# Kernel optimization log

Measured on AMD Instinct MI355X. Metric: run time of the kernel, lower is better.

Reference implementation:

```python
import jax, jax.numpy as jnp
import numpy as np

N_RAYS = 262144
N_BINS = 64          # bin edges per ray
N_IMPORTANCE = 128   # fine samples per ray


def setup_inputs() -> dict:
    key = jax.random.key(0)
    k1, k2, k3 = jax.random.split(key, 3)
    # bins must be sorted along last axis (bin edges): cumsum of positive steps
    steps = jax.random.uniform(k1, (N_RAYS, N_BINS), dtype=jnp.float32) + 0.01
    bins = jnp.cumsum(steps, axis=-1)
    weights = jax.random.uniform(k2, (N_RAYS, N_BINS - 1), dtype=jnp.float32)
    # u plays the role of torch.rand t_vals (deterministic=False path)
    u = jax.random.uniform(k3, (N_RAYS, N_IMPORTANCE), dtype=jnp.float32)
    return {"bins": bins, "weights": weights, "u": u, "n_importance": N_IMPORTANCE}


def reference(bins, weights, u, n_importance):
    # weights: [N, M-1]; bins: [N, M]; u: [N, n_importance]
    weights = weights + 1e-5
    pdf = weights / jnp.sum(weights, axis=-1, keepdims=True)
    cdf = jnp.cumsum(pdf, axis=-1)
    cdf = jnp.concatenate([jnp.zeros_like(cdf[..., :1]), cdf], axis=-1)  # [N, M]

    # batched binary search (torch.searchsorted, right=False -> side='left')
    idx = jax.vmap(lambda c, t: jnp.searchsorted(c, t, side='left'))(
        jax.lax.stop_gradient(cdf), u)                                   # [N, I]
    lower = jnp.maximum(idx - 1, 0)
    upper = jnp.minimum(idx, cdf.shape[-1] - 1)

    cdf_lo = jnp.take_along_axis(cdf, lower, axis=-1)
    cdf_hi = jnp.take_along_axis(cdf, upper, axis=-1)
    bins_lo = jnp.take_along_axis(bins, lower, axis=-1)
    bins_hi = jnp.take_along_axis(bins, upper, axis=-1)

    denom = cdf_hi - cdf_lo
    denom = jnp.where(denom < 1e-5, jnp.ones_like(denom), denom)
    t = (u - cdf_lo) / denom
    samples = bins_lo + t * (bins_hi - bins_lo)                          # [N, I]
    return samples
```

## Files before the change

kernel.cpp:

```cpp
#include <hip/hip_runtime.h>


constexpr int NBINS = 64;
constexpr int NW = NBINS - 1;
constexpr int NIMP = 128;
constexpr int WAVES_PER_BLOCK = 4;
constexpr int RAYS_PER_WAVE = 2;
constexpr int RAYS_PER_BLOCK = WAVES_PER_BLOCK * RAYS_PER_WAVE;

template <int Ctrl, int Rm>
__device__ __forceinline__ float dppterm(float x) {
    return __int_as_float(__builtin_amdgcn_update_dpp(
        0, __float_as_int(x), Ctrl, Rm, 0xF, true));
}

__device__ __forceinline__ float rdlane(float x, int lane) {
    return __int_as_float(__builtin_amdgcn_readlane(__float_as_int(x), lane));
}

__device__ __forceinline__ float bperm_f(float x, int lane_idx) {
    return __int_as_float(
        __builtin_amdgcn_ds_bpermute(lane_idx << 2, __float_as_int(x)));
}

__device__ __forceinline__ float wave_incl_scan(float x) {
    x += dppterm<0x111, 0xF>(x);
    x += dppterm<0x112, 0xF>(x);
    x += dppterm<0x114, 0xF>(x);
    x += dppterm<0x118, 0xF>(x);
    x += dppterm<0x142, 0xA>(x);
    x += dppterm<0x143, 0xC>(x);
    return x;
}

struct Pivots { float c8, c16, c24, c32, c40, c48, c56; };

__device__ __forceinline__ Pivots make_pivots(float cdfv) {
    Pivots p;
    p.c8  = rdlane(cdfv, 8);
    p.c16 = rdlane(cdfv, 16);
    p.c24 = rdlane(cdfv, 24);
    p.c32 = rdlane(cdfv, 32);
    p.c40 = rdlane(cdfv, 40);
    p.c48 = rdlane(cdfv, 48);
    p.c56 = rdlane(cdfv, 56);
    return p;
}

__device__ __forceinline__ float sample_one(float uv, const float* cdf,
                                            float cdfv, float bv,
                                            const Pivots& P)
{
    const int grp = (int)(P.c8 < uv) + (int)(P.c16 < uv) + (int)(P.c24 < uv) +
                    (int)(P.c32 < uv) + (int)(P.c40 < uv) + (int)(P.c48 < uv) +
                    (int)(P.c56 < uv);
    const int pos = grp << 3;

    const float4 g0 = *(const float4*)(cdf + pos);
    const float4 g1 = *(const float4*)(cdf + pos + 4);
    const int cnt = (int)(g0.y < uv) + (int)(g0.z < uv) + (int)(g0.w < uv) +
                    (int)(g1.x < uv) + (int)(g1.y < uv) + (int)(g1.z < uv) +
                    (int)(g1.w < uv);

    const int lower = pos + cnt;
    const int upper = (uv > 0.0f) ? (lower + 1) : 0;

    const float lo  = bperm_f(cdfv, lower);
    const float chi = bperm_f(cdfv, upper);
    const float blo = bperm_f(bv, lower);
    const float bhi = bperm_f(bv, upper);

    float denom = chi - lo;
    denom = (denom < 1e-5f) ? 1.0f : denom;
    const float t = (uv - lo) * __builtin_amdgcn_rcpf(denom);
    return __builtin_fmaf(t, bhi - blo, blo);
}

__global__ __launch_bounds__(256) void sample_pdf_kernel(
    const float* __restrict__ bins,
    const float* __restrict__ weights,
    const float* __restrict__ u,
    float* __restrict__ out,
    int n_rays)
{
    __shared__ alignas(16) float s_cdf[WAVES_PER_BLOCK][RAYS_PER_WAVE][NBINS];

    const int wave = threadIdx.x >> 6;
    const int lane = threadIdx.x & 63;
    const int base = blockIdx.x * RAYS_PER_BLOCK + wave * RAYS_PER_WAVE;
    const uint32_t rA = (uint32_t)min(base,     n_rays - 1);
    const uint32_t rB = (uint32_t)min(base + 1, n_rays - 1);

    const float bvA = bins[rA * NBINS + lane];
    const float bvB = bins[rB * NBINS + lane];
    float wrA = 0.0f, wrB = 0.0f;
    if (lane < NW) {
        wrA = weights[rA * NW + lane];
        wrB = weights[rB * NW + lane];
    }
    const float2 uuA = ((const float2*)u)[rA * (NIMP / 2) + lane];
    const float2 uuB = ((const float2*)u)[rB * (NIMP / 2) + lane];

    asm volatile("" :: "v"(bvA), "v"(bvB), "v"(wrA), "v"(wrB),
                       "v"(uuA.x), "v"(uuA.y), "v"(uuB.x), "v"(uuB.y));

    const float wA = (lane < NW) ? (wrA + 1e-5f) : 0.0f;
    const float wB = (lane < NW) ? (wrB + 1e-5f) : 0.0f;
    const float SA = wave_incl_scan(wA);
    const float SB = wave_incl_scan(wB);
    float cdfvA = (SA - wA) * __builtin_amdgcn_rcpf(rdlane(SA, 63));
    float cdfvB = (SB - wB) * __builtin_amdgcn_rcpf(rdlane(SB, 63));
    if (lane == NBINS - 1) { cdfvA = 1.0f; cdfvB = 1.0f; }

    s_cdf[wave][0][lane] = cdfvA;
    s_cdf[wave][1][lane] = cdfvB;

    const Pivots PA = make_pivots(cdfvA);
    const Pivots PB = make_pivots(cdfvB);

    const float* cA = s_cdf[wave][0];
    const float* cB = s_cdf[wave][1];

    float2 resA, resB;
    resA.x = sample_one(uuA.x, cA, cdfvA, bvA, PA);
    resA.y = sample_one(uuA.y, cA, cdfvA, bvA, PA);
    resB.x = sample_one(uuB.x, cB, cdfvB, bvB, PB);
    resB.y = sample_one(uuB.y, cB, cdfvB, bvB, PB);

    ((float2*)out)[rA * (NIMP / 2) + lane] = resA;
    ((float2*)out)[rB * (NIMP / 2) + lane] = resB;
}

extern "C" void kernel_launch(void* const* d_in, const int* in_sizes, int n_in,
                              void* d_out, int out_size, void* d_ws, size_t ws_size,
                              hipStream_t stream) {
    const float* bins    = (const float*)d_in[0];
    const float* weights = (const float*)d_in[1];
    const float* u       = (const float*)d_in[2];
    float* out = (float*)d_out;

    const int n_rays = in_sizes[0] / NBINS;
    const int grid = (n_rays + RAYS_PER_BLOCK - 1) / RAYS_PER_BLOCK;
    sample_pdf_kernel<<<grid, 256, 0, stream>>>(bins, weights, u, out, n_rays);
}
```

Baseline: 305.5 us.

## Batch LDS and bpermute lookups across samples and enlarge blocks to 1024 threads

The per-sample search is restructured so the coarse pivot search, the LDS window loads and the bpermute gathers for all four samples are issued in separate batched phases. Compiler barriers force each batch to stay together, which lets LDS latency overlap across samples instead of serializing per sample. Blocks grow from 4 to 16 waves with launch bounds of 1024 and a minimum of 8, which may constrain registers. The scheduling barrier on the global loads is removed.

```diff
diff --git a/kernel.cpp b/kernel.cpp
--- a/kernel.cpp
+++ b/kernel.cpp
@@ -4,7 +4,7 @@
 constexpr int NBINS = 64;
 constexpr int NW = NBINS - 1;
 constexpr int NIMP = 128;
-constexpr int WAVES_PER_BLOCK = 4;
+constexpr int WAVES_PER_BLOCK = 16;
 constexpr int RAYS_PER_WAVE = 2;
 constexpr int RAYS_PER_BLOCK = WAVES_PER_BLOCK * RAYS_PER_WAVE;
 
@@ -47,36 +47,13 @@
     return p;
 }
 
-__device__ __forceinline__ float sample_one(float uv, const float* cdf,
-                                            float cdfv, float bv,
-                                            const Pivots& P)
-{
-    const int grp = (int)(P.c8 < uv) + (int)(P.c16 < uv) + (int)(P.c24 < uv) +
-                    (int)(P.c32 < uv) + (int)(P.c40 < uv) + (int)(P.c48 < uv) +
-                    (int)(P.c56 < uv);
-    const int pos = grp << 3;
-
-    const float4 g0 = *(const float4*)(cdf + pos);
-    const float4 g1 = *(const float4*)(cdf + pos + 4);
-    const int cnt = (int)(g0.y < uv) + (int)(g0.z < uv) + (int)(g0.w < uv) +
-                    (int)(g1.x < uv) + (int)(g1.y < uv) + (int)(g1.z < uv) +
-                    (int)(g1.w < uv);
-
-    const int lower = pos + cnt;
-    const int upper = (uv > 0.0f) ? (lower + 1) : 0;
-
-    const float lo  = bperm_f(cdfv, lower);
-    const float chi = bperm_f(cdfv, upper);
-    const float blo = bperm_f(bv, lower);
-    const float bhi = bperm_f(bv, upper);
-
-    float denom = chi - lo;
-    denom = (denom < 1e-5f) ? 1.0f : denom;
-    const float t = (uv - lo) * __builtin_amdgcn_rcpf(denom);
-    return __builtin_fmaf(t, bhi - blo, blo);
+__device__ __forceinline__ int level_a(float uv, const Pivots& P) {
+    return ((int)(P.c8 < uv) + (int)(P.c16 < uv) + (int)(P.c24 < uv) +
+            (int)(P.c32 < uv) + (int)(P.c40 < uv) + (int)(P.c48 < uv) +
+            (int)(P.c56 < uv)) << 3;
 }
 
-__global__ __launch_bounds__(256) void sample_pdf_kernel(
+__global__ __launch_bounds__(1024, 8) void sample_pdf_kernel(
     const float* __restrict__ bins,
     const float* __restrict__ weights,
     const float* __restrict__ u,
@@ -101,9 +78,6 @@
     const float2 uuA = ((const float2*)u)[rA * (NIMP / 2) + lane];
     const float2 uuB = ((const float2*)u)[rB * (NIMP / 2) + lane];
 
-    asm volatile("" :: "v"(bvA), "v"(bvB), "v"(wrA), "v"(wrB),
-                       "v"(uuA.x), "v"(uuA.y), "v"(uuB.x), "v"(uuB.y));
-
     const float wA = (lane < NW) ? (wrA + 1e-5f) : 0.0f;
     const float wB = (lane < NW) ? (wrB + 1e-5f) : 0.0f;
     const float SA = wave_incl_scan(wA);
@@ -121,11 +95,61 @@
     const float* cA = s_cdf[wave][0];
     const float* cB = s_cdf[wave][1];
 
+    const float uv0 = uuA.x, uv1 = uuA.y, uv2 = uuB.x, uv3 = uuB.y;
+
+    const int pos0 = level_a(uv0, PA);
+    const int pos1 = level_a(uv1, PA);
+    const int pos2 = level_a(uv2, PB);
+    const int pos3 = level_a(uv3, PB);
+
+    const float4 w00 = *(const float4*)(cA + pos0);
+    const float4 w01 = *(const float4*)(cA + pos0 + 4);
+    const float4 w10 = *(const float4*)(cA + pos1);
+    const float4 w11 = *(const float4*)(cA + pos1 + 4);
+    const float4 w20 = *(const float4*)(cB + pos2);
+    const float4 w21 = *(const float4*)(cB + pos2 + 4);
+    const float4 w30 = *(const float4*)(cB + pos3);
+    const float4 w31 = *(const float4*)(cB + pos3 + 4);
+    asm volatile("" :: "v"(w00.x), "v"(w01.x), "v"(w10.x), "v"(w11.x),
+                       "v"(w20.x), "v"(w21.x), "v"(w30.x), "v"(w31.x));
+
+    #define CNT(w0_, w1_, uv_) ((int)(w0_.y < uv_) + (int)(w0_.z < uv_) + \
+        (int)(w0_.w < uv_) + (int)(w1_.x < uv_) + (int)(w1_.y < uv_) + \
+        (int)(w1_.z < uv_) + (int)(w1_.w < uv_))
+    const int lo0 = pos0 + CNT(w00, w01, uv0);
+    const int lo1 = pos1 + CNT(w10, w11, uv1);
+    const int lo2 = pos2 + CNT(w20, w21, uv2);
+    const int lo3 = pos3 + CNT(w30, w31, uv3);
+    #undef CNT
+    const int up0 = (uv0 > 0.0f) ? (lo0 + 1) : 0;
+    const int up1 = (uv1 > 0.0f) ? (lo1 + 1) : 0;
+    const int up2 = (uv2 > 0.0f) ? (lo2 + 1) : 0;
+    const int up3 = (uv3 > 0.0f) ? (lo3 + 1) : 0;
+
+    const float l0 = bperm_f(cdfvA, lo0), h0 = bperm_f(cdfvA, up0);
+    const float p0 = bperm_f(bvA,  lo0), q0 = bperm_f(bvA,  up0);
+    const float l1 = bperm_f(cdfvA, lo1), h1 = bperm_f(cdfvA, up1);
+    const float p1 = bperm_f(bvA,  lo1), q1 = bperm_f(bvA,  up1);
+    const float l2 = bperm_f(cdfvB, lo2), h2 = bperm_f(cdfvB, up2);
+    const float p2 = bperm_f(bvB,  lo2), q2 = bperm_f(bvB,  up2);
+    const float l3 = bperm_f(cdfvB, lo3), h3 = bperm_f(cdfvB, up3);
+    const float p3 = bperm_f(bvB,  lo3), q3 = bperm_f(bvB,  up3);
+    asm volatile("" :: "v"(l0), "v"(h0), "v"(p0), "v"(q0),
+                       "v"(l1), "v"(h1), "v"(p1), "v"(q1),
+                       "v"(l2), "v"(h2), "v"(p2), "v"(q2),
+                       "v"(l3), "v"(h3), "v"(p3), "v"(q3));
+
+    #define FINAL(uv_, l_, h_, p_, q_, dst_) { \
+        float den = h_ - l_; \
+        den = (den < 1e-5f) ? 1.0f : den; \
+        const float t = (uv_ - l_) * __builtin_amdgcn_rcpf(den); \
+        dst_ = __builtin_fmaf(t, q_ - p_, p_); }
     float2 resA, resB;
-    resA.x = sample_one(uuA.x, cA, cdfvA, bvA, PA);
-    resA.y = sample_one(uuA.y, cA, cdfvA, bvA, PA);
-    resB.x = sample_one(uuB.x, cB, cdfvB, bvB, PB);
-    resB.y = sample_one(uuB.y, cB, cdfvB, bvB, PB);
+    FINAL(uv0, l0, h0, p0, q0, resA.x);
+    FINAL(uv1, l1, h1, p1, q1, resA.y);
+    FINAL(uv2, l2, h2, p2, q2, resB.x);
+    FINAL(uv3, l3, h3, p3, q3, resB.y);
+    #undef FINAL
 
     ((float2*)out)[rA * (NIMP / 2) + lane] = resA;
     ((float2*)out)[rB * (NIMP / 2) + lane] = resB;
@@ -141,5 +165,5 @@
 
     const int n_rays = in_sizes[0] / NBINS;
     const int grid = (n_rays + RAYS_PER_BLOCK - 1) / RAYS_PER_BLOCK;
-    sample_pdf_kernel<<<grid, 256, 0, stream>>>(bins, weights, u, out, n_rays);
+    sample_pdf_kernel<<<grid, 1024, 0, stream>>>(bins, weights, u, out, n_rays);
 }
```

Measured after the change: 310.7 us. About the same (+1.7%).
